# Kernel tuning notes

Measured on AMD Instinct MI355X. Metric: run time of the kernel, lower is better.

The kernel has to match this reference:

```python
import jax, jax.numpy as jnp
import numpy as np

N, HID, K, L, OUT = 325, 64, 2, 2, 1


def _supports(adj):
    # dual random walk: transposed random-walk matrices D^-1 W (as in original DCRNN)
    S1 = (adj / adj.sum(1, keepdims=True)).T
    adjT = adj.T
    S2 = (adjT / adjT.sum(1, keepdims=True)).T
    return (S1, S2)


def _gconv(x, h, W, b, supports):
    # x: [B, N*in_dim], h: [B, N*HID]
    B = x.shape[0]
    xh = jnp.concatenate([x.reshape(B, N, -1), h.reshape(B, N, -1)], -1)  # [B,N,C]
    C = xh.shape[-1]
    x0 = xh.transpose(1, 2, 0).reshape(N, C * B)  # [N, C*B]
    mats = [x0]
    for S in supports:
        x1 = S @ x0
        mats.append(x1)
        xk2, xk1 = x0, x1
        for _ in range(2, K + 1):
            x2 = 2.0 * (S @ xk1) - xk2
            mats.append(x2)
            xk2, xk1 = xk1, x2
    M = len(mats)  # 2*K + 1 = 5
    xs = jnp.stack(mats, 0).reshape(M, N, C, B).transpose(3, 1, 2, 0).reshape(B * N, C * M)
    return xs @ W + b


def _cell(x, h, Wg, bg, Wc, bc, supports):
    B = x.shape[0]
    val = jax.nn.sigmoid(_gconv(x, h, Wg, bg, supports).reshape(B, N, 2 * HID))
    r, u = jnp.split(val, 2, axis=-1)
    r = r.reshape(B, N * HID)
    u = u.reshape(B, N * HID)
    c = jnp.tanh(_gconv(x, r * h, Wc, bc, supports).reshape(B, N * HID))
    return u * h + (1.0 - u) * c


def setup_inputs() -> dict:
    key = jax.random.key(0)
    ks = jax.random.split(key, 14)
    B, H1 = 64, 13
    return {
        "inputs": jax.random.normal(ks[0], (H1, B, N, 1), jnp.float32),
        "init_state": jax.random.normal(ks[1], (L, B, N * HID), jnp.float32) * 0.1,
        "adj_mx": jax.random.uniform(ks[2], (N, N), jnp.float32, 0.01, 1.0),
        "Wg0": jax.random.normal(ks[3], ((1 + HID) * (2 * K + 1), 2 * HID), jnp.float32) * 0.05,
        "bg0": jnp.ones((2 * HID,), jnp.float32),
        "Wc0": jax.random.normal(ks[4], ((1 + HID) * (2 * K + 1), HID), jnp.float32) * 0.05,
        "bc0": jnp.zeros((HID,), jnp.float32),
        "Wg1": jax.random.normal(ks[5], ((2 * HID) * (2 * K + 1), 2 * HID), jnp.float32) * 0.05,
        "bg1": jnp.ones((2 * HID,), jnp.float32),
        "Wc1": jax.random.normal(ks[6], ((2 * HID) * (2 * K + 1), HID), jnp.float32) * 0.05,
        "bc1": jnp.zeros((HID,), jnp.float32),
        "W_fc": jax.random.normal(ks[7], (HID, OUT), jnp.float32) * 0.1,
        "b_fc": jnp.zeros((OUT,), jnp.float32),
        "teaching_force_ratio": 1,
    }


def reference(inputs, init_state, adj_mx, Wg0, bg0, Wc0, bc0, Wg1, bg1, Wc1, bc1, W_fc, b_fc, teaching_force_ratio):
    H1, B = inputs.shape[0], inputs.shape[1]
    inp = inputs.reshape(H1, B, -1)
    supports = _supports(adj_mx)
    params = ((Wg0, bg0, Wc0, bc0), (Wg1, bg1, Wc1, bc1))

    def step(carry, x_t):
        cur, state = carry
        layer_in = cur
        hs = []
        for l in range(L):
            h_new = _cell(layer_in, state[l], params[l][0], params[l][1], params[l][2], params[l][3], supports)
            layer_in = h_new
            hs.append(h_new)
        state = jnp.stack(hs, 0)
        out = (h_new.reshape(-1, HID) @ W_fc + b_fc).reshape(B, N * OUT)
        # teaching_force_ratio == 1 -> teacher forcing every step (deterministic)
        return (x_t, state), out

    (_, _), outs = jax.lax.scan(step, (inp[0], init_state), inp[1:])
    zero0 = jnp.zeros((1, B, N * OUT), outs.dtype)  # outputs[0] left as zeros, matching torch code
    return jnp.concatenate([zero0, outs], 0)
```

## Files before the change

### kernel.cpp

```cpp
#include <hip/hip_runtime.h>
#include <math.h>

#define NN    325
#define BB    64
#define TT    12
#define NODE  4096
#define KD    352
#define NPADR 384
#define XP    360
#define OBP   72
#define KP0   352
#define KP1   640
#define SB2   512

typedef unsigned short ushort;
typedef __attribute__((ext_vector_type(8))) short short8v;
typedef __attribute__((ext_vector_type(4))) short short4v;
typedef __attribute__((ext_vector_type(4))) float float4v;

static __device__ __forceinline__ ushort f2bf(float f){
  unsigned u = __builtin_bit_cast(unsigned, f);
  u += 0x7fffu + ((u >> 16) & 1u);
  return (ushort)(u >> 16);
}

__global__ void k_sums(const float* __restrict__ adj, float* __restrict__ rs,
                       float* __restrict__ cs){
  __shared__ float red[8];
  int j = blockIdx.x;
  int tid = threadIdx.x, gq = tid >> 6;
  float rv = 0.f, cv = 0.f;
  for (int k = tid; k < NN; k += 256){
    rv += adj[j*NN + k];
    cv += adj[k*NN + j];
  }
  #pragma unroll
  for (int o = 32; o > 0; o >>= 1){
    rv += __shfl_down(rv, o);
    cv += __shfl_down(cv, o);
  }
  if ((tid & 63) == 0){ red[gq] = rv; red[4 + gq] = cv; }
  __syncthreads();
  if (tid == 0){
    rs[j] = red[0]+red[1]+red[2]+red[3];
    cs[j] = red[4]+red[5]+red[6]+red[7];
  }
}

__global__ void k_setup2(const float* __restrict__ adj, const float* __restrict__ rs,
                         const float* __restrict__ cs, const float* __restrict__ inp,
                         const float* __restrict__ init,
                         const float* __restrict__ Wg0, const float* __restrict__ Wc0,
                         const float* __restrict__ Wg1, const float* __restrict__ Wc1,
                         float* __restrict__ Sfp, ushort* __restrict__ Scomb,
                         ushort* __restrict__ Wg0t, ushort* __restrict__ Wc0t,
                         ushort* __restrict__ Wg1t, ushort* __restrict__ Wc1t,
                         float* __restrict__ h0, float* __restrict__ h1,
                         ushort* __restrict__ matsL0, ushort* __restrict__ matsL1){
  int bx = blockIdx.x, t = threadIdx.x;
  if (bx < NN){
    int n = bx, b = t & 63, cq = t >> 6;
    #pragma unroll
    for (int ii = 0; ii < 16; ++ii){
      int c = cq*16 + ii;
      float h0v = init[(size_t)(b*NN + n)*64 + c];
      float h1v = init[(size_t)BB*NN*64 + (size_t)(b*NN + n)*64 + c];
      h0[(size_t)n*NODE + c*64 + b] = h0v;
      h1[(size_t)n*NODE + c*64 + b] = h1v;
      matsL0[((size_t)(1 + c)*NN + n)*64 + b]  = f2bf(h0v);
      matsL1[((size_t)c*NN + n)*64 + b]        = f2bf(h0v);
      matsL1[((size_t)(64 + c)*NN + n)*64 + b] = f2bf(h1v);
    }
    if (t < 64)
      matsL0[(size_t)n*64 + t] = f2bf(inp[(size_t)t*NN + n]);
  }
  for (int idx = bx*256 + t; idx < 2*NN*NN; idx += SB2*256){
    int s = idx / (NN*NN), rem = idx - s*(NN*NN);
    int i = rem / NN, j = rem - i*NN;
    float v = s ? adj[i*NN + j]/cs[j] : adj[j*NN + i]/rs[j];
    Sfp[idx] = v;
    Scomb[(size_t)(2*s)*NPADR*KD + (size_t)i*KD + j] = f2bf(v);
  }
  {
    const float* Ws[4] = { Wg0, Wc0, Wg1, Wc1 };
    ushort* Wts[4]     = { Wg0t, Wc0t, Wg1t, Wc1t };
    const int Cs[4] = { 65, 65, 128, 128 };
    const int Os[4] = { 128, 64, 128, 64 };
    const int Kp[4] = { KP0, KP0, KP1, KP1 };
    for (int q = 0; q < 4; ++q){
      int total = Os[q]*Kp[q];
      for (int idx = bx*256 + t; idx < total; idx += SB2*256){
        int o = idx / Kp[q], k = idx - o*Kp[q];
        int m = k / Cs[q], c = k - m*Cs[q];
        Wts[q][idx] = f2bf(m < 5 ? Ws[q][(c*5 + m)*Os[q] + o] : 0.f);
      }
    }
  }
}

__global__ __launch_bounds__(256) void k_s2(const float* __restrict__ Sfp,
                                            ushort* __restrict__ Scomb){
  __shared__ ushort X[64][XP];
  int jt = blockIdx.x, rh2 = blockIdx.y, s = blockIdx.z;
  int t = threadIdx.x, w = t >> 6, r = t & 15, g = (t >> 4) & 3;
  const float* S = Sfp + (size_t)s*NN*NN;
  for (int idx = t; idx < KD*8; idx += 256){
    int k = idx >> 3, j0 = (idx & 7)*8;
    #pragma unroll
    for (int i = 0; i < 8; ++i){
      int j = j0 + i, col = jt*64 + j;
      float v = (k < NN && col < NN) ? S[(size_t)k*NN + col] : 0.f;
      X[j][k] = f2bf(v);
    }
  }
  __syncthreads();
  const ushort* A = Scomb + (size_t)(2*s)*NPADR*KD + (size_t)(rh2*192)*KD;
  float4v acc[3][4];
  #pragma unroll
  for (int i = 0; i < 3; ++i)
    #pragma unroll
    for (int q = 0; q < 4; ++q) acc[i][q] = (float4v){0.f,0.f,0.f,0.f};
  for (int kc = 0; kc < KD/32; ++kc){
    short8v a[3], bbv[4];
    #pragma unroll
    for (int mt = 0; mt < 3; ++mt)
      a[mt] = *(const short8v*)&A[(size_t)((w*3 + mt)*16 + r)*KD + kc*32 + g*8];
    #pragma unroll
    for (int nt = 0; nt < 4; ++nt)
      bbv[nt] = *(const short8v*)&X[nt*16 + r][kc*32 + g*8];
    #pragma unroll
    for (int mt = 0; mt < 3; ++mt)
      #pragma unroll
      for (int nt = 0; nt < 4; ++nt)
        acc[mt][nt] = __builtin_amdgcn_mfma_f32_16x16x32_bf16(a[mt], bbv[nt], acc[mt][nt], 0, 0, 0);
  }
  ushort* dst = Scomb + (size_t)(2*s + 1)*NPADR*KD;
  #pragma unroll
  for (int mt = 0; mt < 3; ++mt){
    int node0 = rh2*192 + (w*3 + mt)*16 + g*4;
    #pragma unroll
    for (int nt = 0; nt < 4; ++nt){
      int col = nt*16 + r, jg = jt*64 + col;
      #pragma unroll
      for (int i = 0; i < 4; ++i){
        int n = node0 + i;
        if (n < NN && jg < NN)
          dst[(size_t)n*KD + jg] = f2bf(2.f*acc[mt][nt][i] - (n == jg ? 1.f : 0.f));
      }
    }
  }
}

struct Seg {
  const ushort* sm;
  const float*  sf;
  ushort* dm;  int C,  cs0, cd0;
  ushort* dm2; int C2, cd2;
};
struct DiffA {
  const ushort* Sc;
  Seg seg[3];
  int e0, e1, nch;
};

__global__ __launch_bounds__(256, 3) void k_diffN(DiffA da){
  __shared__ ushort X[64][XP];
  ushort (*OB)[OBP] = (ushort (*)[OBP])&X[0][0];
  int lin = blockIdx.x;
  int cu = (lin >> 6)*8 + (lin & 7);
  if (cu >= da.nch) return;
  int sub = (lin >> 3) & 7;
  const int y = sub >> 2, m = sub & 3;
  Seg sg; int u;
  if (cu < da.e0){ sg = da.seg[0]; u = cu; }
  else if (cu < da.e1){ sg = da.seg[1]; u = cu - da.e0; }
  else { sg = da.seg[2]; u = cu - da.e1; }
  int t = threadIdx.x, w = t >> 6;
  int r = t & 15, g = (t >> 4) & 3;

  if (sg.sm){
    const ushort* src = sg.sm + (size_t)(sg.cs0 + u)*NN*64;
    int nb = t >> 3, b0 = (t & 7)*8;
    int swz = (t & 3) << 3;
    const short8v vz = {0,0,0,0,0,0,0,0};
    short8v v[11];
    #pragma unroll
    for (int j = 0; j < 11; ++j){
      int n = j*32 + nb;
      v[j] = (n < NN) ? *(const short8v*)&src[(size_t)n*64 + b0] : vz;
    }
    #pragma unroll
    for (int j = 0; j < 11; ++j){
      int col = (j*32 + nb) ^ swz;
      #pragma unroll
      for (int i = 0; i < 8; ++i) X[b0 + i][col] = (ushort)v[j][i];
    }
  } else {
    for (int j = 0; j < 22; ++j){
      int idx = j*256 + t;
      int b = idx / 88, n4 = (idx - b*88)*4;
      int swz = ((b >> 3) & 3) << 3;
      ushort us[4];
      #pragma unroll
      for (int i = 0; i < 4; ++i)
        us[i] = (n4 + i < NN) ? f2bf(sg.sf[(size_t)b*NN + n4 + i]) : (ushort)0;
      short4v pk; pk[0]=(short)us[0]; pk[1]=(short)us[1]; pk[2]=(short)us[2]; pk[3]=(short)us[3];
      *(short4v*)&X[b][n4 ^ swz] = pk;
      #pragma unroll
      for (int i = 0; i < 4; ++i)
        if (n4 + i < NN) sg.dm[(size_t)(n4 + i)*64 + b] = us[i];
    }
  }
  __syncthreads();

  const ushort* S = da.Sc + ((size_t)m*NPADR + (size_t)y*192)*KD;
  int swr[4];
  #pragma unroll
  for (int nt = 0; nt < 4; ++nt)
    swr[nt] = ((nt*2 + (r >> 3)) & 3) << 3;
  float4v acc[3][4];
  #pragma unroll
  for (int i = 0; i < 3; ++i)
    #pragma unroll
    for (int q = 0; q < 4; ++q) acc[i][q] = (float4v){0.f,0.f,0.f,0.f};
  for (int kc = 0; kc < KD/32; ++kc){
    short8v a[3], bbv[4];
    #pragma unroll
    for (int mt = 0; mt < 3; ++mt)
      a[mt] = *(const short8v*)&S[(size_t)((w*3 + mt)*16 + r)*KD + kc*32 + g*8];
    #pragma unroll
    for (int nt = 0; nt < 4; ++nt)
      bbv[nt] = *(const short8v*)&X[nt*16 + r][(kc*32 + g*8) ^ swr[nt]];
    #pragma unroll
    for (int mt = 0; mt < 3; ++mt)
      #pragma unroll
      for (int nt = 0; nt < 4; ++nt)
        acc[mt][nt] = __builtin_amdgcn_mfma_f32_16x16x32_bf16(a[mt], bbv[nt], acc[mt][nt], 0, 0, 0);
  }

  __syncthreads();
  #pragma unroll
  for (int mt = 0; mt < 3; ++mt){
    int lr0 = (w*3 + mt)*16 + g*4;
    #pragma unroll
    for (int nt = 0; nt < 4; ++nt){
      int col = nt*16 + r;
      #pragma unroll
      for (int i = 0; i < 4; ++i)
        OB[lr0 + i][col] = f2bf(acc[mt][nt][i]);
    }
  }
  __syncthreads();
  {
    ushort* dst = sg.dm + (size_t)((1 + m)*sg.C + sg.cd0 + u)*NN*64;
    ushort* dst2 = sg.dm2 ? sg.dm2 + (size_t)((1 + m)*sg.C2 + sg.cd2 + u)*NN*64
                          : nullptr;
    int n0 = y*192;
    int lr = t >> 3, q = (t & 7)*8;
    #pragma unroll
    for (int it = 0; it < 6; ++it){
      int row = it*32 + lr;
      int n = n0 + row;
      if (n < NN){
        short8v vv = *(short8v*)&OB[row][q];
        *(short8v*)&dst[(size_t)n*64 + q] = vv;
        if (dst2) *(short8v*)&dst2[(size_t)n*64 + q] = vv;
      }
    }
  }
}

struct WgD {
  const ushort* mats; const ushort* Wt; const float* bias;
  float* h; float* uu;
  ushort* dstA; ushort* dstB;
  const float* Wfc; const float* bfc; float* outp;
  int KPAD; int MODE;
};

template<int KPAD>
static __device__ __forceinline__ void wg_body(
    const WgD& d, int n, int oy, ushort (*XT)[XP], float* fcbuf)
{
  constexpr int NST = (KPAD > 352) ? 2 : 1;
  constexpr int KH  = (KPAD > 352) ? 320 : KPAD;
  constexpr int NCH = KH/32;
  int t = threadIdx.x, w = t >> 6;
  int r = t & 15, g = (t >> 4) & 3;
  const bool fc = (d.MODE == 1) && (d.outp != nullptr);
  if (fc && t < 64) fcbuf[t] = 0.f;

  float4v acc[4];
  #pragma unroll
  for (int nt = 0; nt < 4; ++nt) acc[nt] = (float4v){0.f,0.f,0.f,0.f};

  int kk0 = t >> 3, b0 = (t & 7)*8;
  int swz = (t & 3) << 3;
  int swr[4];
  #pragma unroll
  for (int nt = 0; nt < 4; ++nt)
    swr[nt] = ((nt*2 + (r >> 3)) & 3) << 3;
  #pragma unroll
  for (int st = 0; st < NST; ++st){
    int kbase = st*KH;
    if (st) __syncthreads();
    short8v v[NCH];
    #pragma unroll
    for (int j = 0; j < NCH; ++j)
      v[j] = *(const short8v*)&d.mats[((size_t)(kbase + j*32 + kk0)*NN + n)*64 + b0];
    #pragma unroll
    for (int j = 0; j < NCH; ++j){
      int col = (j*32 + kk0) ^ swz;
      #pragma unroll
      for (int i = 0; i < 8; ++i) XT[b0 + i][col] = (ushort)v[j][i];
    }
    __syncthreads();
    for (int kc = 0; kc < NCH; ++kc){
      short8v a0 = *(const short8v*)&d.Wt[(size_t)(oy*64 + w*16 + r)*KPAD + kbase + kc*32 + g*8];
      short8v bbv[4];
      #pragma unroll
      for (int nt = 0; nt < 4; ++nt)
        bbv[nt] = *(const short8v*)&XT[nt*16 + r][(kc*32 + g*8) ^ swr[nt]];
      #pragma unroll
      for (int nt = 0; nt < 4; ++nt)
        acc[nt] = __builtin_amdgcn_mfma_f32_16x16x32_bf16(a0, bbv[nt], acc[nt], 0, 0, 0);
    }
  }

  __syncthreads();
  #pragma unroll
  for (int nt = 0; nt < 4; ++nt){
    int b2 = nt*16 + r;
    float p = 0.f;
    #pragma unroll
    for (int i = 0; i < 4; ++i){
      int o = w*16 + g*4 + i;
      float vv = acc[nt][i] + d.bias[oy*64 + o];
      if (d.MODE == 0){
        float sg = 1.f/(1.f + expf(-vv));
        if (oy == 0) XT[o][b2] = f2bf(sg * d.h[(size_t)n*NODE + o*64 + b2]);
        else         d.uu[(size_t)n*NODE + o*64 + b2] = sg;
      } else {
        float cv = tanhf(vv);
        size_t idx = (size_t)n*NODE + o*64 + b2;
        float uv = d.uu[idx];
        float hn = uv*d.h[idx] + (1.f - uv)*cv;
        d.h[idx] = hn;
        XT[o][b2] = f2bf(hn);
        if (fc) p += hn * d.Wfc[o];
      }
    }
    if (fc) atomicAdd(&fcbuf[b2], p);
  }
  __syncthreads();
  if (d.MODE == 1 || oy == 0){
    int o = t >> 2, q = (t & 3)*16;
    short8v v0 = *(short8v*)&XT[o][q];
    short8v v1 = *(short8v*)&XT[o][q + 8];
    ushort* dl = d.dstA + ((size_t)o*NN + n)*64 + q;
    *(short8v*)&dl[0] = v0;
    *(short8v*)&dl[8] = v1;
    if (d.dstB){
      ushort* dl2 = d.dstB + ((size_t)o*NN + n)*64 + q;
      *(short8v*)&dl2[0] = v0;
      *(short8v*)&dl2[8] = v1;
    }
  }
  if (fc && t < 64)
    d.outp[(size_t)t*NN + n] = fcbuf[t] + d.bfc[0];
}

__global__ __launch_bounds__(256) void k_wg2(WgD d0, int n0, WgD d1){
  __shared__ ushort XT[64][XP];
  __shared__ float fcbuf[64];
  const bool first = (blockIdx.x < (unsigned)n0);
  WgD d = first ? d0 : d1;
  int n = first ? blockIdx.x : blockIdx.x - n0;
  int oy = blockIdx.y;
  if (d.MODE == 1 && oy) return;
  if (d.KPAD == 352) wg_body<352>(d, n, oy, XT, fcbuf);
  else               wg_body<640>(d, n, oy, XT, fcbuf);
}

extern "C" void kernel_launch(void* const* d_in, const int* in_sizes, int n_in,
                              void* d_out, int out_size, void* d_ws, size_t ws_size,
                              hipStream_t stream){
  const float* inp  = (const float*)d_in[0];
  const float* init = (const float*)d_in[1];
  const float* adj  = (const float*)d_in[2];
  const float* Wg0  = (const float*)d_in[3];
  const float* bg0  = (const float*)d_in[4];
  const float* Wc0  = (const float*)d_in[5];
  const float* bc0  = (const float*)d_in[6];
  const float* Wg1  = (const float*)d_in[7];
  const float* bg1  = (const float*)d_in[8];
  const float* Wc1  = (const float*)d_in[9];
  const float* bc1  = (const float*)d_in[10];
  const float* Wfc  = (const float*)d_in[11];
  const float* bfc  = (const float*)d_in[12];
  (void)in_sizes; (void)n_in; (void)out_size; (void)ws_size;

  char* p = (char*)d_ws;
  auto alloc = [&](size_t bytes) -> void* {
    void* q = (void*)p; p += (bytes + 255) & ~(size_t)255; return q;
  };
  ushort* Scomb  = (ushort*)alloc((size_t)4*NPADR*KD*2);
  float*  Sfp    = (float*)alloc((size_t)2*NN*NN*4);
  ushort* Wg0t   = (ushort*)alloc((size_t)128*KP0*2);
  ushort* Wc0t   = (ushort*)alloc((size_t)64*KP0*2);
  ushort* Wg1t   = (ushort*)alloc((size_t)128*KP1*2);
  ushort* Wc1t   = (ushort*)alloc((size_t)64*KP1*2);
  float*  rs     = (float*)alloc(512*4);
  float*  cs     = (float*)alloc(512*4);
  float*  h0     = (float*)alloc((size_t)NN*NODE*4);
  float*  h1     = (float*)alloc((size_t)NN*NODE*4);
  float*  uu0    = (float*)alloc((size_t)NN*NODE*4);
  float*  uu1    = (float*)alloc((size_t)NN*NODE*4);
  ushort* matsL0 = (ushort*)alloc((size_t)KP0*NN*64*2);
  ushort* matsL1 = (ushort*)alloc((size_t)KP1*NN*64*2);
  float* out = (float*)d_out;

  hipMemsetAsync(out, 0, (size_t)BB*NN*4, stream);
  hipMemsetAsync(matsL0 + (size_t)325*NN*64, 0, (size_t)(KP0 - 325)*NN*64*2, stream);
  hipMemsetAsync(Scomb, 0, (size_t)4*NPADR*KD*2, stream);

  k_sums<<<NN, 256, 0, stream>>>(adj, rs, cs);
  k_setup2<<<SB2, 256, 0, stream>>>(adj, rs, cs, inp, init, Wg0, Wc0, Wg1, Wc1,
                                    Sfp, Scomb, Wg0t, Wc0t, Wg1t, Wc1t,
                                    h0, h1, matsL0, matsL1);
  k_s2<<<dim3(6, 2, 2), 256, 0, stream>>>(Sfp, Scomb);

  auto diffGrid = [](int nch){ return ((nch + 7)/8)*64; };

  Seg segH0d = { matsL0, nullptr, matsL0, 65, 1, 1, matsL1, 128, 0 };
  Seg segH1  = { matsL1, nullptr, matsL1, 128, 64, 64, nullptr, 0, 0 };
  Seg segRh0 = { matsL0, nullptr, matsL0, 65, 1, 1, nullptr, 0, 0 };
  Seg segRh1 = { matsL1, nullptr, matsL1, 128, 64, 64, nullptr, 0, 0 };

  WgD wg_g0 = { matsL0, Wg0t, bg0, h0, uu0, matsL0 + (size_t)1*NN*64, nullptr,
                nullptr, nullptr, nullptr, KP0, 0 };
  WgD wg_c0 = { matsL0, Wc0t, bc0, h0, uu0, matsL0 + (size_t)1*NN*64, matsL1,
                nullptr, nullptr, nullptr, KP0, 1 };
  WgD wg_g1 = { matsL1, Wg1t, bg1, h1, uu1, matsL1 + (size_t)64*NN*64, nullptr,
                nullptr, nullptr, nullptr, KP1, 0 };

  for (int t = 0; t <= TT; ++t){
    if (t < TT){
      Seg segX = { nullptr, inp + (size_t)t*BB*NN, matsL0, 65, 0, 0, nullptr, 0, 0 };
      DiffA da = { Scomb, { segH0d, segH1, segX }, 64, 128, 129 };
      k_diffN<<<diffGrid(129), 256, 0, stream>>>(da);
    } else {
      DiffA da = { Scomb, { segH0d, segH1, segH1 }, 64, 128, 128 };
      k_diffN<<<diffGrid(128), 256, 0, stream>>>(da);
    }
    if (t == 0)
      k_wg2<<<dim3(NN, 2), 256, 0, stream>>>(wg_g0, NN, wg_g0);
    else if (t < TT)
      k_wg2<<<dim3(2*NN, 2), 256, 0, stream>>>(wg_g0, NN, wg_g1);
    else
      k_wg2<<<dim3(NN, 2), 256, 0, stream>>>(wg_g1, NN, wg_g1);
    if (t == 0){
      DiffA da = { Scomb, { segRh0, segRh0, segRh0 }, 64, 64, 64 };
      k_diffN<<<diffGrid(64), 256, 0, stream>>>(da);
    } else if (t < TT){
      DiffA da = { Scomb, { segRh0, segRh1, segRh1 }, 64, 128, 128 };
      k_diffN<<<diffGrid(128), 256, 0, stream>>>(da);
    } else {
      DiffA da = { Scomb, { segRh1, segRh1, segRh1 }, 64, 64, 64 };
      k_diffN<<<diffGrid(64), 256, 0, stream>>>(da);
    }
    WgD wg_c1 = { matsL1, Wc1t, bc1, h1, uu1, matsL1 + (size_t)64*NN*64, nullptr,
                  Wfc, bfc, out + (size_t)t*BB*NN, KP1, 1 };
    if (t == 0)
      k_wg2<<<dim3(NN, 1), 256, 0, stream>>>(wg_c0, NN, wg_c0);
    else if (t < TT)
      k_wg2<<<dim3(2*NN, 1), 256, 0, stream>>>(wg_c0, NN, wg_c1);
    else
      k_wg2<<<dim3(NN, 1), 256, 0, stream>>>(wg_c1, NN, wg_c1);
  }
}
```

Before: 1.481 ms.

## Process two channels per diffusion block with prefetch, add nontemporal memory ops

```diff
diff --git a/kernel.cpp b/kernel.cpp
--- a/kernel.cpp
+++ b/kernel.cpp
@@ -167,104 +167,133 @@
   __shared__ ushort X[64][XP];
   ushort (*OB)[OBP] = (ushort (*)[OBP])&X[0][0];
   int lin = blockIdx.x;
-  int cu = (lin >> 6)*8 + (lin & 7);
-  if (cu >= da.nch) return;
+  int cup = (lin >> 6)*8 + (lin & 7);
+  int npairs = (da.nch + 1) >> 1;
+  if (cup >= npairs) return;
   int sub = (lin >> 3) & 7;
   const int y = sub >> 2, m = sub & 3;
-  Seg sg; int u;
-  if (cu < da.e0){ sg = da.seg[0]; u = cu; }
-  else if (cu < da.e1){ sg = da.seg[1]; u = cu - da.e0; }
-  else { sg = da.seg[2]; u = cu - da.e1; }
   int t = threadIdx.x, w = t >> 6;
   int r = t & 15, g = (t >> 4) & 3;
-
-  if (sg.sm){
-    const ushort* src = sg.sm + (size_t)(sg.cs0 + u)*NN*64;
-    int nb = t >> 3, b0 = (t & 7)*8;
-    int swz = (t & 3) << 3;
-    const short8v vz = {0,0,0,0,0,0,0,0};
-    short8v v[11];
+  int nb = t >> 3, b0 = (t & 7)*8;
+  int swz = (t & 3) << 3;
+
+  const ushort* S = da.Sc + ((size_t)m*NPADR + (size_t)y*192)*KD;
+  int swr[4];
+  #pragma unroll
+  for (int nt = 0; nt < 4; ++nt)
+    swr[nt] = ((nt*2 + (r >> 3)) & 3) << 3;
+
+  int c0 = cup*2;
+  const int ncl = (c0 + 1 < da.nch) ? 2 : 1;
+
+  auto resolve = [&](int cu, Seg& sg, int& u){
+    if (cu < da.e0){ sg = da.seg[0]; u = cu; }
+    else if (cu < da.e1){ sg = da.seg[1]; u = cu - da.e0; }
+    else { sg = da.seg[2]; u = cu - da.e1; }
+  };
+
+  const short8v vz = {0,0,0,0,0,0,0,0};
+  short8v v[11];
+  Seg sgc, sgn; int uc, un;
+  resolve(c0, sgc, uc);
+  if (sgc.sm){
+    const ushort* src = sgc.sm + (size_t)(sgc.cs0 + uc)*NN*64;
     #pragma unroll
     for (int j = 0; j < 11; ++j){
       int n = j*32 + nb;
-      v[j] = (n < NN) ? *(const short8v*)&src[(size_t)n*64 + b0] : vz;
-    }
-    #pragma unroll
-    for (int j = 0; j < 11; ++j){
-      int col = (j*32 + nb) ^ swz;
-      #pragma unroll
-      for (int i = 0; i < 8; ++i) X[b0 + i][col] = (ushort)v[j][i];
-    }
-  } else {
-    for (int j = 0; j < 22; ++j){
-      int idx = j*256 + t;
-      int b = idx / 88, n4 = (idx - b*88)*4;
-      int swz = ((b >> 3) & 3) << 3;
-      ushort us[4];
-      #pragma unroll
-      for (int i = 0; i < 4; ++i)
-        us[i] = (n4 + i < NN) ? f2bf(sg.sf[(size_t)b*NN + n4 + i]) : (ushort)0;
-      short4v pk; pk[0]=(short)us[0]; pk[1]=(short)us[1]; pk[2]=(short)us[2]; pk[3]=(short)us[3];
-      *(short4v*)&X[b][n4 ^ swz] = pk;
-      #pragma unroll
-      for (int i = 0; i < 4; ++i)
-        if (n4 + i < NN) sg.dm[(size_t)(n4 + i)*64 + b] = us[i];
-    }
-  }
-  __syncthreads();
-
-  const ushort* S = da.Sc + ((size_t)m*NPADR + (size_t)y*192)*KD;
-  int swr[4];
-  #pragma unroll
-  for (int nt = 0; nt < 4; ++nt)
-    swr[nt] = ((nt*2 + (r >> 3)) & 3) << 3;
-  float4v acc[3][4];
-  #pragma unroll
-  for (int i = 0; i < 3; ++i)
-    #pragma unroll
-    for (int q = 0; q < 4; ++q) acc[i][q] = (float4v){0.f,0.f,0.f,0.f};
-  for (int kc = 0; kc < KD/32; ++kc){
-    short8v a[3], bbv[4];
-    #pragma unroll
-    for (int mt = 0; mt < 3; ++mt)
-      a[mt] = *(const short8v*)&S[(size_t)((w*3 + mt)*16 + r)*KD + kc*32 + g*8];
-    #pragma unroll
-    for (int nt = 0; nt < 4; ++nt)
-      bbv[nt] = *(const short8v*)&X[nt*16 + r][(kc*32 + g*8) ^ swr[nt]];
-    #pragma unroll
-    for (int mt = 0; mt < 3; ++mt)
+      v[j] = (n < NN) ? __builtin_nontemporal_load((const short8v*)&src[(size_t)n*64 + b0]) : vz;
+    }
+  }
+
+  for (int ci = 0; ci < ncl; ++ci){
+    if (ci){ sgc = sgn; uc = un; __syncthreads(); }
+    if (sgc.sm){
+      #pragma unroll
+      for (int j = 0; j < 11; ++j){
+        int col = (j*32 + nb) ^ swz;
+        #pragma unroll
+        for (int i = 0; i < 8; ++i) X[b0 + i][col] = (ushort)v[j][i];
+      }
+    } else {
+      for (int j = 0; j < 22; ++j){
+        int idx = j*256 + t;
+        int b = idx / 88, n4 = (idx - b*88)*4;
+        int swz2 = ((b >> 3) & 3) << 3;
+        ushort us[4];
+        #pragma unroll
+        for (int i = 0; i < 4; ++i)
+          us[i] = (n4 + i < NN) ? f2bf(sgc.sf[(size_t)b*NN + n4 + i]) : (ushort)0;
+        short4v pk; pk[0]=(short)us[0]; pk[1]=(short)us[1]; pk[2]=(short)us[2]; pk[3]=(short)us[3];
+        *(short4v*)&X[b][n4 ^ swz2] = pk;
+        #pragma unroll
+        for (int i = 0; i < 4; ++i)
+          if (n4 + i < NN)
+            __builtin_nontemporal_store(us[i], &sgc.dm[(size_t)(n4 + i)*64 + b]);
+      }
+    }
+    __syncthreads();
+
+    if (ci == 0 && ncl == 2){
+      resolve(c0 + 1, sgn, un);
+      if (sgn.sm){
+        const ushort* src = sgn.sm + (size_t)(sgn.cs0 + un)*NN*64;
+        #pragma unroll
+        for (int j = 0; j < 11; ++j){
+          int n = j*32 + nb;
+          v[j] = (n < NN) ? __builtin_nontemporal_load((const short8v*)&src[(size_t)n*64 + b0]) : vz;
+        }
+      }
+    }
+
+    float4v acc[3][4];
+    #pragma unroll
+    for (int i = 0; i < 3; ++i)
+      #pragma unroll
+      for (int q = 0; q < 4; ++q) acc[i][q] = (float4v){0.f,0.f,0.f,0.f};
+    for (int kc = 0; kc < KD/32; ++kc){
+      short8v a[3], bbv[4];
+      #pragma unroll
+      for (int mt = 0; mt < 3; ++mt)
+        a[mt] = *(const short8v*)&S[(size_t)((w*3 + mt)*16 + r)*KD + kc*32 + g*8];
       #pragma unroll
       for (int nt = 0; nt < 4; ++nt)
-        acc[mt][nt] = __builtin_amdgcn_mfma_f32_16x16x32_bf16(a[mt], bbv[nt], acc[mt][nt], 0, 0, 0);
-  }
-
-  __syncthreads();
-  #pragma unroll
-  for (int mt = 0; mt < 3; ++mt){
-    int lr0 = (w*3 + mt)*16 + g*4;
-    #pragma unroll
-    for (int nt = 0; nt < 4; ++nt){
-      int col = nt*16 + r;
-      #pragma unroll
-      for (int i = 0; i < 4; ++i)
-        OB[lr0 + i][col] = f2bf(acc[mt][nt][i]);
-    }
-  }
-  __syncthreads();
-  {
-    ushort* dst = sg.dm + (size_t)((1 + m)*sg.C + sg.cd0 + u)*NN*64;
-    ushort* dst2 = sg.dm2 ? sg.dm2 + (size_t)((1 + m)*sg.C2 + sg.cd2 + u)*NN*64
-                          : nullptr;
-    int n0 = y*192;
-    int lr = t >> 3, q = (t & 7)*8;
-    #pragma unroll
-    for (int it = 0; it < 6; ++it){
-      int row = it*32 + lr;
-      int n = n0 + row;
-      if (n < NN){
-        short8v vv = *(short8v*)&OB[row][q];
-        *(short8v*)&dst[(size_t)n*64 + q] = vv;
-        if (dst2) *(short8v*)&dst2[(size_t)n*64 + q] = vv;
+        bbv[nt] = *(const short8v*)&X[nt*16 + r][(kc*32 + g*8) ^ swr[nt]];
+      #pragma unroll
+      for (int mt = 0; mt < 3; ++mt)
+        #pragma unroll
+        for (int nt = 0; nt < 4; ++nt)
+          acc[mt][nt] = __builtin_amdgcn_mfma_f32_16x16x32_bf16(a[mt], bbv[nt], acc[mt][nt], 0, 0, 0);
+    }
+
+    __syncthreads();
+    #pragma unroll
+    for (int mt = 0; mt < 3; ++mt){
+      int lr0 = (w*3 + mt)*16 + g*4;
+      #pragma unroll
+      for (int nt = 0; nt < 4; ++nt){
+        int col = nt*16 + r;
+        #pragma unroll
+        for (int i = 0; i < 4; ++i)
+          OB[lr0 + i][col] = f2bf(acc[mt][nt][i]);
+      }
+    }
+    __syncthreads();
+    {
+      ushort* dst = sgc.dm + (size_t)((1 + m)*sgc.C + sgc.cd0 + uc)*NN*64;
+      ushort* dst2 = sgc.dm2 ? sgc.dm2 + (size_t)((1 + m)*sgc.C2 + sgc.cd2 + uc)*NN*64
+                             : nullptr;
+      int n0 = y*192;
+      int lr = t >> 3, q = (t & 7)*8;
+      #pragma unroll
+      for (int it = 0; it < 6; ++it){
+        int row = it*32 + lr;
+        int n = n0 + row;
+        if (n < NN){
+          short8v vv = *(short8v*)&OB[row][q];
+          __builtin_nontemporal_store(vv, (short8v*)&dst[(size_t)n*64 + q]);
+          if (dst2)
+            __builtin_nontemporal_store(vv, (short8v*)&dst2[(size_t)n*64 + q]);
+        }
       }
     }
   }
@@ -307,7 +336,8 @@
     short8v v[NCH];
     #pragma unroll
     for (int j = 0; j < NCH; ++j)
-      v[j] = *(const short8v*)&d.mats[((size_t)(kbase + j*32 + kk0)*NN + n)*64 + b0];
+      v[j] = __builtin_nontemporal_load(
+          (const short8v*)&d.mats[((size_t)(kbase + j*32 + kk0)*NN + n)*64 + b0]);
     #pragma unroll
     for (int j = 0; j < NCH; ++j){
       int col = (j*32 + kk0) ^ swz;
@@ -339,11 +369,11 @@
       if (d.MODE == 0){
         float sg = 1.f/(1.f + expf(-vv));
         if (oy == 0) XT[o][b2] = f2bf(sg * d.h[(size_t)n*NODE + o*64 + b2]);
-        else         d.uu[(size_t)n*NODE + o*64 + b2] = sg;
+        else         __builtin_nontemporal_store(sg, &d.uu[(size_t)n*NODE + o*64 + b2]);
       } else {
         float cv = tanhf(vv);
         size_t idx = (size_t)n*NODE + o*64 + b2;
-        float uv = d.uu[idx];
+        float uv = __builtin_nontemporal_load(&d.uu[idx]);
         float hn = uv*d.h[idx] + (1.f - uv)*cv;
         d.h[idx] = hn;
         XT[o][b2] = f2bf(hn);
@@ -358,12 +388,12 @@
     short8v v0 = *(short8v*)&XT[o][q];
     short8v v1 = *(short8v*)&XT[o][q + 8];
     ushort* dl = d.dstA + ((size_t)o*NN + n)*64 + q;
-    *(short8v*)&dl[0] = v0;
-    *(short8v*)&dl[8] = v1;
+    __builtin_nontemporal_store(v0, (short8v*)&dl[0]);
+    __builtin_nontemporal_store(v1, (short8v*)&dl[8]);
     if (d.dstB){
       ushort* dl2 = d.dstB + ((size_t)o*NN + n)*64 + q;
-      *(short8v*)&dl2[0] = v0;
-      *(short8v*)&dl2[8] = v1;
+      __builtin_nontemporal_store(v0, (short8v*)&dl2[0]);
+      __builtin_nontemporal_store(v1, (short8v*)&dl2[8]);
     }
   }
   if (fc && t < 64)
@@ -430,7 +460,7 @@
                                     h0, h1, matsL0, matsL1);
   k_s2<<<dim3(6, 2, 2), 256, 0, stream>>>(Sfp, Scomb);
 
-  auto diffGrid = [](int nch){ return ((nch + 7)/8)*64; };
+  auto diffGrid = [](int nch){ int np = (nch + 1) >> 1; return ((np + 7)/8)*64; };
 
   Seg segH0d = { matsL0, nullptr, matsL0, 65, 1, 1, matsL1, 128, 0 };
   Seg segH1  = { matsL1, nullptr, matsL1, 128, 64, 64, nullptr, 0, 0 };
```

After: 2.002 ms. +35.1%, slower.

## Compute two diffusion supports per block and fuse gate halves into one block

Applied to the files above, without the earlier changes.

```diff
diff --git a/kernel.cpp b/kernel.cpp
--- a/kernel.cpp
+++ b/kernel.cpp
@@ -167,10 +167,10 @@
   __shared__ ushort X[64][XP];
   ushort (*OB)[OBP] = (ushort (*)[OBP])&X[0][0];
   int lin = blockIdx.x;
-  int cu = (lin >> 6)*8 + (lin & 7);
+  int cu = (lin >> 5)*8 + (lin & 7);
   if (cu >= da.nch) return;
-  int sub = (lin >> 3) & 7;
-  const int y = sub >> 2, m = sub & 3;
+  int sub = (lin >> 3) & 3;
+  const int y = sub >> 1, mp = sub & 1;
   Seg sg; int u;
   if (cu < da.e0){ sg = da.seg[0]; u = cu; }
   else if (cu < da.e1){ sg = da.seg[1]; u = cu - da.e0; }
@@ -199,13 +199,13 @@
     for (int j = 0; j < 22; ++j){
       int idx = j*256 + t;
       int b = idx / 88, n4 = (idx - b*88)*4;
-      int swz = ((b >> 3) & 3) << 3;
+      int swz2 = ((b >> 3) & 3) << 3;
       ushort us[4];
       #pragma unroll
       for (int i = 0; i < 4; ++i)
         us[i] = (n4 + i < NN) ? f2bf(sg.sf[(size_t)b*NN + n4 + i]) : (ushort)0;
       short4v pk; pk[0]=(short)us[0]; pk[1]=(short)us[1]; pk[2]=(short)us[2]; pk[3]=(short)us[3];
-      *(short4v*)&X[b][n4 ^ swz] = pk;
+      *(short4v*)&X[b][n4 ^ swz2] = pk;
       #pragma unroll
       for (int i = 0; i < 4; ++i)
         if (n4 + i < NN) sg.dm[(size_t)(n4 + i)*64 + b] = us[i];
@@ -213,50 +213,61 @@
   }
   __syncthreads();
 
-  const ushort* S = da.Sc + ((size_t)m*NPADR + (size_t)y*192)*KD;
+  const ushort* S0 = da.Sc + ((size_t)(mp*2 + 0)*NPADR + (size_t)y*192)*KD;
+  const ushort* S1 = da.Sc + ((size_t)(mp*2 + 1)*NPADR + (size_t)y*192)*KD;
   int swr[4];
   #pragma unroll
   for (int nt = 0; nt < 4; ++nt)
     swr[nt] = ((nt*2 + (r >> 3)) & 3) << 3;
-  float4v acc[3][4];
+  float4v acc0[3][4], acc1[3][4];
   #pragma unroll
   for (int i = 0; i < 3; ++i)
     #pragma unroll
-    for (int q = 0; q < 4; ++q) acc[i][q] = (float4v){0.f,0.f,0.f,0.f};
+    for (int q = 0; q < 4; ++q){
+      acc0[i][q] = (float4v){0.f,0.f,0.f,0.f};
+      acc1[i][q] = (float4v){0.f,0.f,0.f,0.f};
+    }
   for (int kc = 0; kc < KD/32; ++kc){
-    short8v a[3], bbv[4];
-    #pragma unroll
-    for (int mt = 0; mt < 3; ++mt)
-      a[mt] = *(const short8v*)&S[(size_t)((w*3 + mt)*16 + r)*KD + kc*32 + g*8];
+    short8v a0[3], a1[3], bbv[4];
+    #pragma unroll
+    for (int mt = 0; mt < 3; ++mt){
+      size_t rowo = (size_t)((w*3 + mt)*16 + r)*KD + kc*32 + g*8;
+      a0[mt] = *(const short8v*)&S0[rowo];
+      a1[mt] = *(const short8v*)&S1[rowo];
+    }
     #pragma unroll
     for (int nt = 0; nt < 4; ++nt)
       bbv[nt] = *(const short8v*)&X[nt*16 + r][(kc*32 + g*8) ^ swr[nt]];
     #pragma unroll
     for (int mt = 0; mt < 3; ++mt)
       #pragma unroll
-      for (int nt = 0; nt < 4; ++nt)
-        acc[mt][nt] = __builtin_amdgcn_mfma_f32_16x16x32_bf16(a[mt], bbv[nt], acc[mt][nt], 0, 0, 0);
+      for (int nt = 0; nt < 4; ++nt){
+        acc0[mt][nt] = __builtin_amdgcn_mfma_f32_16x16x32_bf16(a0[mt], bbv[nt], acc0[mt][nt], 0, 0, 0);
+        acc1[mt][nt] = __builtin_amdgcn_mfma_f32_16x16x32_bf16(a1[mt], bbv[nt], acc1[mt][nt], 0, 0, 0);
+      }
   }
 
   __syncthreads();
-  #pragma unroll
-  for (int mt = 0; mt < 3; ++mt){
-    int lr0 = (w*3 + mt)*16 + g*4;
-    #pragma unroll
-    for (int nt = 0; nt < 4; ++nt){
-      int col = nt*16 + r;
-      #pragma unroll
-      for (int i = 0; i < 4; ++i)
-        OB[lr0 + i][col] = f2bf(acc[mt][nt][i]);
-    }
-  }
-  __syncthreads();
-  {
+  int n0 = y*192;
+  int lr = t >> 3, q = (t & 7)*8;
+  #pragma unroll
+  for (int mi = 0; mi < 2; ++mi){
+    #pragma unroll
+    for (int mt = 0; mt < 3; ++mt){
+      int lr0 = (w*3 + mt)*16 + g*4;
+      #pragma unroll
+      for (int nt = 0; nt < 4; ++nt){
+        int col = nt*16 + r;
+        #pragma unroll
+        for (int i = 0; i < 4; ++i)
+          OB[lr0 + i][col] = f2bf(mi ? acc1[mt][nt][i] : acc0[mt][nt][i]);
+      }
+    }
+    __syncthreads();
+    int m = mp*2 + mi;
     ushort* dst = sg.dm + (size_t)((1 + m)*sg.C + sg.cd0 + u)*NN*64;
     ushort* dst2 = sg.dm2 ? sg.dm2 + (size_t)((1 + m)*sg.C2 + sg.cd2 + u)*NN*64
                           : nullptr;
-    int n0 = y*192;
-    int lr = t >> 3, q = (t & 7)*8;
     #pragma unroll
     for (int it = 0; it < 6; ++it){
       int row = it*32 + lr;
@@ -267,6 +278,7 @@
         if (dst2) *(short8v*)&dst2[(size_t)n*64 + q] = vv;
       }
     }
+    if (mi == 0) __syncthreads();
   }
 }
 
@@ -280,19 +292,23 @@
 
 template<int KPAD>
 static __device__ __forceinline__ void wg_body(
-    const WgD& d, int n, int oy, ushort (*XT)[XP], float* fcbuf)
+    const WgD& d, int n, ushort (*XT)[XP], float* fcbuf)
 {
   constexpr int NST = (KPAD > 352) ? 2 : 1;
   constexpr int KH  = (KPAD > 352) ? 320 : KPAD;
   constexpr int NCH = KH/32;
   int t = threadIdx.x, w = t >> 6;
   int r = t & 15, g = (t >> 4) & 3;
+  const bool m0 = (d.MODE == 0);
   const bool fc = (d.MODE == 1) && (d.outp != nullptr);
   if (fc && t < 64) fcbuf[t] = 0.f;
 
-  float4v acc[4];
-  #pragma unroll
-  for (int nt = 0; nt < 4; ++nt) acc[nt] = (float4v){0.f,0.f,0.f,0.f};
+  float4v acc0[4], acc1[4];
+  #pragma unroll
+  for (int nt = 0; nt < 4; ++nt){
+    acc0[nt] = (float4v){0.f,0.f,0.f,0.f};
+    acc1[nt] = (float4v){0.f,0.f,0.f,0.f};
+  }
 
   int kk0 = t >> 3, b0 = (t & 7)*8;
   int swz = (t & 3) << 3;
@@ -316,14 +332,21 @@
     }
     __syncthreads();
     for (int kc = 0; kc < NCH; ++kc){
-      short8v a0 = *(const short8v*)&d.Wt[(size_t)(oy*64 + w*16 + r)*KPAD + kbase + kc*32 + g*8];
+      short8v a0 = *(const short8v*)&d.Wt[(size_t)(w*16 + r)*KPAD + kbase + kc*32 + g*8];
+      short8v a1;
+      if (m0)
+        a1 = *(const short8v*)&d.Wt[(size_t)((w + 4)*16 + r)*KPAD + kbase + kc*32 + g*8];
       short8v bbv[4];
       #pragma unroll
       for (int nt = 0; nt < 4; ++nt)
         bbv[nt] = *(const short8v*)&XT[nt*16 + r][(kc*32 + g*8) ^ swr[nt]];
       #pragma unroll
       for (int nt = 0; nt < 4; ++nt)
-        acc[nt] = __builtin_amdgcn_mfma_f32_16x16x32_bf16(a0, bbv[nt], acc[nt], 0, 0, 0);
+        acc0[nt] = __builtin_amdgcn_mfma_f32_16x16x32_bf16(a0, bbv[nt], acc0[nt], 0, 0, 0);
+      if (m0)
+        #pragma unroll
+        for (int nt = 0; nt < 4; ++nt)
+          acc1[nt] = __builtin_amdgcn_mfma_f32_16x16x32_bf16(a1, bbv[nt], acc1[nt], 0, 0, 0);
     }
   }
 
@@ -335,11 +358,10 @@
     #pragma unroll
     for (int i = 0; i < 4; ++i){
       int o = w*16 + g*4 + i;
-      float vv = acc[nt][i] + d.bias[oy*64 + o];
-      if (d.MODE == 0){
-        float sg = 1.f/(1.f + expf(-vv));
-        if (oy == 0) XT[o][b2] = f2bf(sg * d.h[(size_t)n*NODE + o*64 + b2]);
-        else         d.uu[(size_t)n*NODE + o*64 + b2] = sg;
+      float vv = acc0[nt][i] + d.bias[o];
+      if (m0){
+        float sg2 = 1.f/(1.f + expf(-vv));
+        XT[o][b2] = f2bf(sg2 * d.h[(size_t)n*NODE + o*64 + b2]);
       } else {
         float cv = tanhf(vv);
         size_t idx = (size_t)n*NODE + o*64 + b2;
@@ -352,8 +374,20 @@
     }
     if (fc) atomicAdd(&fcbuf[b2], p);
   }
+  if (m0){
+    #pragma unroll
+    for (int nt = 0; nt < 4; ++nt){
+      int b2 = nt*16 + r;
+      #pragma unroll
+      for (int i = 0; i < 4; ++i){
+        int o = w*16 + g*4 + i;
+        float vv = acc1[nt][i] + d.bias[64 + o];
+        d.uu[(size_t)n*NODE + o*64 + b2] = 1.f/(1.f + expf(-vv));
+      }
+    }
+  }
   __syncthreads();
-  if (d.MODE == 1 || oy == 0){
+  {
     int o = t >> 2, q = (t & 3)*16;
     short8v v0 = *(short8v*)&XT[o][q];
     short8v v1 = *(short8v*)&XT[o][q + 8];
@@ -376,10 +410,8 @@
   const bool first = (blockIdx.x < (unsigned)n0);
   WgD d = first ? d0 : d1;
   int n = first ? blockIdx.x : blockIdx.x - n0;
-  int oy = blockIdx.y;
-  if (d.MODE == 1 && oy) return;
-  if (d.KPAD == 352) wg_body<352>(d, n, oy, XT, fcbuf);
-  else               wg_body<640>(d, n, oy, XT, fcbuf);
+  if (d.KPAD == 352) wg_body<352>(d, n, XT, fcbuf);
+  else               wg_body<640>(d, n, XT, fcbuf);
 }
 
 extern "C" void kernel_launch(void* const* d_in, const int* in_sizes, int n_in,
@@ -430,7 +462,7 @@
                                     h0, h1, matsL0, matsL1);
   k_s2<<<dim3(6, 2, 2), 256, 0, stream>>>(Sfp, Scomb);
 
-  auto diffGrid = [](int nch){ return ((nch + 7)/8)*64; };
+  auto diffGrid = [](int nch){ return ((nch + 7)/8)*32; };
 
   Seg segH0d = { matsL0, nullptr, matsL0, 65, 1, 1, matsL1, 128, 0 };
   Seg segH1  = { matsL1, nullptr, matsL1, 128, 64, 64, nullptr, 0, 0 };
@@ -454,11 +486,11 @@
       k_diffN<<<diffGrid(128), 256, 0, stream>>>(da);
     }
     if (t == 0)
-      k_wg2<<<dim3(NN, 2), 256, 0, stream>>>(wg_g0, NN, wg_g0);
+      k_wg2<<<NN, 256, 0, stream>>>(wg_g0, NN, wg_g0);
     else if (t < TT)
-      k_wg2<<<dim3(2*NN, 2), 256, 0, stream>>>(wg_g0, NN, wg_g1);
+      k_wg2<<<2*NN, 256, 0, stream>>>(wg_g0, NN, wg_g1);
     else
-      k_wg2<<<dim3(NN, 2), 256, 0, stream>>>(wg_g1, NN, wg_g1);
+      k_wg2<<<NN, 256, 0, stream>>>(wg_g1, NN, wg_g1);
     if (t == 0){
       DiffA da = { Scomb, { segRh0, segRh0, segRh0 }, 64, 64, 64 };
       k_diffN<<<diffGrid(64), 256, 0, stream>>>(da);
@@ -472,10 +504,10 @@
     WgD wg_c1 = { matsL1, Wc1t, bc1, h1, uu1, matsL1 + (size_t)64*NN*64, nullptr,
                   Wfc, bfc, out + (size_t)t*BB*NN, KP1, 1 };
     if (t == 0)
-      k_wg2<<<dim3(NN, 1), 256, 0, stream>>>(wg_c0, NN, wg_c0);
+      k_wg2<<<NN, 256, 0, stream>>>(wg_c0, NN, wg_c0);
     else if (t < TT)
-      k_wg2<<<dim3(2*NN, 1), 256, 0, stream>>>(wg_c0, NN, wg_c1);
+      k_wg2<<<2*NN, 256, 0, stream>>>(wg_c0, NN, wg_c1);
     else
-      k_wg2<<<dim3(NN, 1), 256, 0, stream>>>(wg_c1, NN, wg_c1);
-  }
-}
+      k_wg2<<<NN, 256, 0, stream>>>(wg_c1, NN, wg_c1);
+  }
+}
```

Measured after the change: 1.580 ms. 6.7% more time.
